# Optimization experiments

Measured on AMD Instinct MI355X. Metric: run time of the kernel, lower is better.

Reference implementation:

```python
import jax, jax.numpy as jnp
import numpy as np

NH = 8
DIM = 512
NP = 1024
MNP = 4096
BS = 4
TOPK = 32


def setup_inputs() -> dict:
    key = jax.random.key(0)
    ks = jax.random.split(key, 10)
    q = jax.random.normal(ks[0], (NP, BS, DIM), dtype=jnp.float32)
    k = jax.random.normal(ks[1], (MNP, BS, DIM), dtype=jnp.float32)
    v = jax.random.normal(ks[2], (MNP, BS, DIM), dtype=jnp.float32)
    rns_indices = jax.random.randint(ks[3], (BS, NP, TOPK), 0, MNP)
    s = 0.02
    W1 = jax.random.normal(ks[4], (DIM, DIM), dtype=jnp.float32) * s
    b1 = jnp.zeros((DIM,), dtype=jnp.float32)
    W2 = jax.random.normal(ks[5], (DIM, DIM), dtype=jnp.float32) * s
    b2 = jnp.zeros((DIM,), dtype=jnp.float32)
    W3 = jax.random.normal(ks[6], (DIM, DIM), dtype=jnp.float32) * s
    b3 = jnp.zeros((DIM,), dtype=jnp.float32)
    return {"q": q, "k": k, "v": v, "rns_indices": rns_indices,
            "W1": W1, "b1": b1, "W2": W2, "b2": b2, "W3": W3, "b3": b3}


def reference(q, k, v, rns_indices, W1, b1, W2, b2, W3, b3):
    np_, bs, dim = q.shape
    mnp = k.shape[0]
    nh = NH
    dh = dim // nh
    # seq-first -> batch-first, linear projections (torch Linear: x @ W.T + b)
    qh = (jnp.einsum('nbd,ed->bne', q, W1) + b1).reshape(bs, np_, nh, dh)
    kh = (jnp.einsum('mbd,ed->bme', k, W2) + b2).reshape(bs, mnp, nh, dh)
    vh = (jnp.einsum('mbd,ed->bme', v, W3) + b3).reshape(bs, mnp, nh, dh)
    # dense scores: [bs, nh, np, mnp]
    w = jnp.einsum('bnhd,bmhd->bhnm', qh, kh) / jnp.sqrt(jnp.asarray(dh, w_dtype := qh.dtype))
    # scatter-built neighbor mask: [bs, np, mnp] (shared across heads)
    b_idx = jnp.arange(bs)[:, None, None]
    n_idx = jnp.arange(np_)[None, :, None]
    mask = jnp.zeros((bs, np_, mnp), dtype=w.dtype).at[b_idx, n_idx, rns_indices].set(1.0)
    mask = mask[:, None, :, :]  # broadcast over heads
    w = w * mask + (-1e9) * (1.0 - mask)
    w = jax.nn.softmax(w, axis=3)
    out = jnp.einsum('bhnm,bmhd->nbhd', w, vh).reshape(np_, bs, dim)
    return out
```

## Files before the change

kernel.cpp:

```cpp
#include <hip/hip_runtime.h>
#include <hip/hip_bf16.h>
#include <stdint.h>

#define NH   8
#define DIM  512
#define NP   1024
#define MNP  4096
#define BS   4
#define TOPK 32
#define DH   64

typedef __attribute__((ext_vector_type(8))) short bf16x8;
typedef __attribute__((ext_vector_type(4))) float f32x4;

__device__ __forceinline__ unsigned short f2bf(float f) {
    union { float f; unsigned u; } x; x.f = f;
    unsigned r = x.u + 0x7FFFu + ((x.u >> 16) & 1u);
    return (unsigned short)(r >> 16);
}
__device__ __forceinline__ float bf2f(unsigned short h) {
    union { unsigned u; float f; } x; x.u = ((unsigned)h) << 16;
    return x.f;
}

__global__ void cvt_f32_bf16(const float* __restrict__ src,
                             unsigned short* __restrict__ dst, int n) {
    int i = (blockIdx.x * blockDim.x + threadIdx.x) * 4;
    if (i + 3 < n) {
        float4 v = *(const float4*)(src + i);
        ushort4 o;
        o.x = f2bf(v.x); o.y = f2bf(v.y); o.z = f2bf(v.z); o.w = f2bf(v.w);
        *(ushort4*)(dst + i) = o;
    } else {
        for (int j = i; j < n; j++) dst[j] = f2bf(src[j]);
    }
}

#define BM 128
#define BN 128
#define BK 64
#define LDT 72

__global__ __launch_bounds__(256, 2)
void proj_gemm(const float* __restrict__ A, const unsigned short* __restrict__ W,
               const float* __restrict__ bias, unsigned short* __restrict__ C) {
    __shared__ unsigned short As[BM * LDT];
    __shared__ unsigned short Bs[BN * LDT];

    const int tid  = threadIdx.x;
    const int bm   = blockIdx.y * BM;
    const int bn   = blockIdx.x * BN;
    const int wave = tid >> 6;
    const int lane = tid & 63;
    const int wm   = (wave & 1) * 64;
    const int wn   = (wave >> 1) * 64;
    const int l16  = lane & 15;
    const int quad = lane >> 4;

    f32x4 acc[4][4] = {};

    const int a_c4 = (tid & 15) * 4;
    const int a_r0 = tid >> 4;
    const int b_c8 = (tid & 7) * 8;
    const int b_r0 = tid >> 3;

    for (int k0 = 0; k0 < 512; k0 += BK) {
        __syncthreads();
#pragma unroll
        for (int rr = 0; rr < 8; rr++) {
            int row = a_r0 + rr * 16;
            float4 v = *(const float4*)(A + (size_t)(bm + row) * 512 + k0 + a_c4);
            ushort4 o;
            o.x = f2bf(v.x); o.y = f2bf(v.y); o.z = f2bf(v.z); o.w = f2bf(v.w);
            *(ushort4*)(&As[row * LDT + a_c4]) = o;
        }
#pragma unroll
        for (int rr = 0; rr < 4; rr++) {
            int row = b_r0 + rr * 32;
            uint4 p = *(const uint4*)(W + (size_t)(bn + row) * 512 + k0 + b_c8);
            *(uint4*)(&Bs[row * LDT + b_c8]) = p;
        }
        __syncthreads();
#pragma unroll
        for (int kk = 0; kk < BK; kk += 32) {
            bf16x8 af[4], bfr[4];
#pragma unroll
            for (int i = 0; i < 4; i++) {
                af[i]  = *(const bf16x8*)(&As[(wm + i * 16 + l16) * LDT + kk + quad * 8]);
                bfr[i] = *(const bf16x8*)(&Bs[(wn + i * 16 + l16) * LDT + kk + quad * 8]);
            }
#pragma unroll
            for (int i = 0; i < 4; i++)
#pragma unroll
                for (int j = 0; j < 4; j++)
                    acc[i][j] = __builtin_amdgcn_mfma_f32_16x16x32_bf16(
                        af[i], bfr[j], acc[i][j], 0, 0, 0);
        }
    }
#pragma unroll
    for (int i = 0; i < 4; i++) {
        int row = bm + wm + i * 16 + quad * 4;
#pragma unroll
        for (int j = 0; j < 4; j++) {
            int col = bn + wn + j * 16 + l16;
            float bv = bias[col];
#pragma unroll
            for (int r = 0; r < 4; r++)
                C[(size_t)(row + r) * 512 + col] = f2bf(acc[i][j][r] + bv);
        }
    }
}

__global__ __launch_bounds__(256)
void attn_kernel(const unsigned short* __restrict__ Qh,
                 const unsigned short* __restrict__ Kh,
                 const unsigned short* __restrict__ Vh,
                 const int* __restrict__ rns,
                 float* __restrict__ out) {
    __shared__ float sq[NH * 72];
    __shared__ int   sidx[TOPK];
    __shared__ int   srow[TOPK];
    __shared__ float sval[TOPK];
    __shared__ float ss[TOPK][NH];
    __shared__ float sw[TOPK][NH];

    const int bid = blockIdx.x;
    const int n = bid >> 2;
    const int b = bid & 3;
    const int tid = threadIdx.x;

    if (tid < TOPK) {
        int mi = rns[((b * NP + n) * TOPK) + tid];
        sidx[tid] = mi;
        srow[tid] = (mi * BS + b) * DIM;
    }
    {
        const unsigned short* qrow = Qh + (size_t)(n * BS + b) * DIM;
        unsigned int u = *(const unsigned int*)(qrow + tid * 2);
        int e0 = tid * 2;
        sq[(e0 >> 6) * 72 + (e0 & 63)]     = bf2f((unsigned short)(u & 0xffff));
        sq[(e0 >> 6) * 72 + ((e0 + 1) & 63)] = bf2f((unsigned short)(u >> 16));
    }
    __syncthreads();
    if (tid < TOPK) {
        float v = 1.0f;
        int me = sidx[tid];
        for (int j = 0; j < tid; j++)
            if (sidx[j] == me) v = 0.0f;
        sval[tid] = v;
    }
    __syncthreads();
    {
        const int i = tid >> 3;
        const int h = tid & 7;
        const unsigned short* krow = Kh + srow[i] + h * DH;
        const float* qh = sq + h * 72;
        float acc = 0.f;
#pragma unroll
        for (int d = 0; d < DH; d += 8) {
            uint4 kv = *(const uint4*)(krow + d);
            acc += qh[d + 0] * bf2f((unsigned short)(kv.x & 0xffff))
                 + qh[d + 1] * bf2f((unsigned short)(kv.x >> 16))
                 + qh[d + 2] * bf2f((unsigned short)(kv.y & 0xffff))
                 + qh[d + 3] * bf2f((unsigned short)(kv.y >> 16))
                 + qh[d + 4] * bf2f((unsigned short)(kv.z & 0xffff))
                 + qh[d + 5] * bf2f((unsigned short)(kv.z >> 16))
                 + qh[d + 6] * bf2f((unsigned short)(kv.w & 0xffff))
                 + qh[d + 7] * bf2f((unsigned short)(kv.w >> 16));
        }
        ss[i][h] = (sval[i] > 0.f) ? acc * 0.125f : -1e30f;
    }
    __syncthreads();
    if (tid < NH) {
        const int h = tid;
        float m = -1e30f;
        for (int i = 0; i < TOPK; i++) m = fmaxf(m, ss[i][h]);
        float s = 0.f;
        for (int i = 0; i < TOPK; i++) {
            float e = __expf(ss[i][h] - m);
            sw[i][h] = e; s += e;
        }
        float inv = 1.0f / s;
        for (int i = 0; i < TOPK; i++) sw[i][h] *= inv;
    }
    __syncthreads();
    {
        const int e0 = tid * 2;
        const int h = e0 >> 6;
        float a0 = 0.f, a1 = 0.f;
#pragma unroll 8
        for (int i = 0; i < TOPK; i++) {
            float w = sw[i][h];
            unsigned int vv = *(const unsigned int*)(Vh + srow[i] + e0);
            a0 += w * bf2f((unsigned short)(vv & 0xffff));
            a1 += w * bf2f((unsigned short)(vv >> 16));
        }
        float2* o = (float2*)(out + (size_t)(n * BS + b) * DIM + e0);
        *o = make_float2(a0, a1);
    }
}

extern "C" void kernel_launch(void* const* d_in, const int* in_sizes, int n_in,
                              void* d_out, int out_size, void* d_ws, size_t ws_size,
                              hipStream_t stream) {
    const float* q  = (const float*)d_in[0];
    const float* k  = (const float*)d_in[1];
    const float* v  = (const float*)d_in[2];
    const int* rns  = (const int*)d_in[3];
    const float* W1 = (const float*)d_in[4];
    const float* b1 = (const float*)d_in[5];
    const float* W2 = (const float*)d_in[6];
    const float* b2 = (const float*)d_in[7];
    const float* W3 = (const float*)d_in[8];
    const float* b3 = (const float*)d_in[9];
    float* out = (float*)d_out;

    unsigned short* ws  = (unsigned short*)d_ws;
    unsigned short* Wb1 = ws;
    unsigned short* Wb2 = Wb1 + 262144;
    unsigned short* Wb3 = Wb2 + 262144;
    unsigned short* Qh  = Wb3 + 262144;
    unsigned short* Kh  = Qh  + 2097152;
    unsigned short* Vh  = Kh  + 8388608;

    cvt_f32_bf16<<<256, 256, 0, stream>>>(W1, Wb1, 262144);
    cvt_f32_bf16<<<256, 256, 0, stream>>>(W2, Wb2, 262144);
    cvt_f32_bf16<<<256, 256, 0, stream>>>(W3, Wb3, 262144);

    dim3 blk(256);
    proj_gemm<<<dim3(4, 32),  blk, 0, stream>>>(q, Wb1, b1, Qh);
    proj_gemm<<<dim3(4, 128), blk, 0, stream>>>(k, Wb2, b2, Kh);
    proj_gemm<<<dim3(4, 128), blk, 0, stream>>>(v, Wb3, b3, Vh);

    attn_kernel<<<NP * BS, 256, 0, stream>>>(Qh, Kh, Vh, rns, out);
}
```

Before: 204.3 us.

## Pre-convert activations to bf16, batch projections, async LDS loads, shuffle softmax

Measured after the change: 198.7 us. 1.03x faster.

```diff
diff --git a/kernel.cpp b/kernel.cpp
--- a/kernel.cpp
+++ b/kernel.cpp
@@ -1,5 +1,4 @@
 #include <hip/hip_runtime.h>
-#include <hip/hip_bf16.h>
 #include <stdint.h>
 
 #define NH   8
@@ -10,46 +9,64 @@
 #define TOPK 32
 #define DH   64
 
+typedef unsigned short u16;
 typedef __attribute__((ext_vector_type(8))) short bf16x8;
 typedef __attribute__((ext_vector_type(4))) float f32x4;
 
-__device__ __forceinline__ unsigned short f2bf(float f) {
+__device__ __forceinline__ u16 f2bf(float f) {
     union { float f; unsigned u; } x; x.f = f;
     unsigned r = x.u + 0x7FFFu + ((x.u >> 16) & 1u);
-    return (unsigned short)(r >> 16);
-}
-__device__ __forceinline__ float bf2f(unsigned short h) {
+    return (u16)(r >> 16);
+}
+__device__ __forceinline__ float bf2f(u16 h) {
     union { unsigned u; float f; } x; x.u = ((unsigned)h) << 16;
     return x.f;
 }
 
-__global__ void cvt_f32_bf16(const float* __restrict__ src,
-                             unsigned short* __restrict__ dst, int n) {
-    int i = (blockIdx.x * blockDim.x + threadIdx.x) * 4;
-    if (i + 3 < n) {
-        float4 v = *(const float4*)(src + i);
-        ushort4 o;
-        o.x = f2bf(v.x); o.y = f2bf(v.y); o.z = f2bf(v.z); o.w = f2bf(v.w);
-        *(ushort4*)(dst + i) = o;
+__device__ __forceinline__ void async16(const void* g, void* l) {
+    __builtin_amdgcn_global_load_lds(
+        (const __attribute__((address_space(1))) unsigned int*)g,
+        (__attribute__((address_space(3))) unsigned int*)l, 16, 0, 0);
+}
+
+__global__ void cvt_all(const float* __restrict__ W1, const float* __restrict__ W2,
+                        const float* __restrict__ W3, const float* __restrict__ q,
+                        const float* __restrict__ k,  const float* __restrict__ v,
+                        u16* __restrict__ wall, u16* __restrict__ act) {
+    size_t i = ((size_t)blockIdx.x * 256 + threadIdx.x) * 4;
+    const float* s; u16* d;
+    if (i < 786432) {
+        d = wall + i;
+        s = (i < 262144) ? W1 + i : (i < 524288) ? W2 + (i - 262144) : W3 + (i - 524288);
     } else {
-        for (int j = i; j < n; j++) dst[j] = f2bf(src[j]);
-    }
-}
-
-#define BM 128
-#define BN 128
-#define BK 64
-#define LDT 72
+        size_t j = i - 786432;
+        d = act + j;
+        s = (j < 2097152) ? q + j : (j < 10485760) ? k + (j - 2097152) : v + (j - 10485760);
+    }
+    float4 val = *(const float4*)s;
+    ushort4 o;
+    o.x = f2bf(val.x); o.y = f2bf(val.y); o.z = f2bf(val.z); o.w = f2bf(val.w);
+    *(ushort4*)d = o;
+}
 
 __global__ __launch_bounds__(256, 2)
-void proj_gemm(const float* __restrict__ A, const unsigned short* __restrict__ W,
-               const float* __restrict__ bias, unsigned short* __restrict__ C) {
-    __shared__ unsigned short As[BM * LDT];
-    __shared__ unsigned short Bs[BN * LDT];
+void proj_gemm(const u16* __restrict__ act, const u16* __restrict__ wall,
+               const float* __restrict__ b1, const float* __restrict__ b2,
+               const float* __restrict__ b3, u16* __restrict__ outall) {
+    __shared__ u16 As[128 * 64];
+    __shared__ u16 Bs[128 * 64];
+
+    const int z = blockIdx.z;
+    if (z == 0 && blockIdx.y >= 32) return;
+    const size_t aoff = (z == 0) ? 0u : (z == 1) ? 2097152u : 10485760u;
+    const u16* A = act + aoff;
+    const u16* W = wall + (size_t)z * 262144;
+    const float* bias = (z == 0) ? b1 : (z == 1) ? b2 : b3;
+    u16* C = outall + aoff;
 
     const int tid  = threadIdx.x;
-    const int bm   = blockIdx.y * BM;
-    const int bn   = blockIdx.x * BN;
+    const int bm   = blockIdx.y * 128;
+    const int bn   = blockIdx.x * 128;
     const int wave = tid >> 6;
     const int lane = tid & 63;
     const int wm   = (wave & 1) * 64;
@@ -57,37 +74,29 @@
     const int l16  = lane & 15;
     const int quad = lane >> 4;
 
+    const int srow = lane >> 3;
+    const int scol = (lane & 7) * 8;
+
     f32x4 acc[4][4] = {};
 
-    const int a_c4 = (tid & 15) * 4;
-    const int a_r0 = tid >> 4;
-    const int b_c8 = (tid & 7) * 8;
-    const int b_r0 = tid >> 3;
-
-    for (int k0 = 0; k0 < 512; k0 += BK) {
+    for (int k0 = 0; k0 < 512; k0 += 64) {
         __syncthreads();
 #pragma unroll
-        for (int rr = 0; rr < 8; rr++) {
-            int row = a_r0 + rr * 16;
-            float4 v = *(const float4*)(A + (size_t)(bm + row) * 512 + k0 + a_c4);
-            ushort4 o;
-            o.x = f2bf(v.x); o.y = f2bf(v.y); o.z = f2bf(v.z); o.w = f2bf(v.w);
-            *(ushort4*)(&As[row * LDT + a_c4]) = o;
-        }
-#pragma unroll
-        for (int rr = 0; rr < 4; rr++) {
-            int row = b_r0 + rr * 32;
-            uint4 p = *(const uint4*)(W + (size_t)(bn + row) * 512 + k0 + b_c8);
-            *(uint4*)(&Bs[row * LDT + b_c8]) = p;
+        for (int r = 0; r < 4; r++) {
+            int row = wave * 32 + r * 8;
+            async16(A + (size_t)(bm + row + srow) * 512 + k0 + scol,
+                    &As[row * 64 + lane * 8]);
+            async16(W + (size_t)(bn + row + srow) * 512 + k0 + scol,
+                    &Bs[row * 64 + lane * 8]);
         }
         __syncthreads();
 #pragma unroll
-        for (int kk = 0; kk < BK; kk += 32) {
+        for (int kk = 0; kk < 64; kk += 32) {
             bf16x8 af[4], bfr[4];
 #pragma unroll
             for (int i = 0; i < 4; i++) {
-                af[i]  = *(const bf16x8*)(&As[(wm + i * 16 + l16) * LDT + kk + quad * 8]);
-                bfr[i] = *(const bf16x8*)(&Bs[(wn + i * 16 + l16) * LDT + kk + quad * 8]);
+                af[i]  = *(const bf16x8*)(&As[(wm + i * 16 + l16) * 64 + kk + quad * 8]);
+                bfr[i] = *(const bf16x8*)(&Bs[(wn + i * 16 + l16) * 64 + kk + quad * 8]);
             }
 #pragma unroll
             for (int i = 0; i < 4; i++)
@@ -112,22 +121,21 @@
 }
 
 __global__ __launch_bounds__(256)
-void attn_kernel(const unsigned short* __restrict__ Qh,
-                 const unsigned short* __restrict__ Kh,
-                 const unsigned short* __restrict__ Vh,
-                 const int* __restrict__ rns,
+void attn_kernel(const u16* __restrict__ Qh, const u16* __restrict__ Kh,
+                 const u16* __restrict__ Vh, const int* __restrict__ rns,
                  float* __restrict__ out) {
     __shared__ float sq[NH * 72];
     __shared__ int   sidx[TOPK];
     __shared__ int   srow[TOPK];
     __shared__ float sval[TOPK];
-    __shared__ float ss[TOPK][NH];
-    __shared__ float sw[TOPK][NH];
+    __shared__ float ss[TOPK][9];
+    __shared__ float sw[TOPK][9];
 
     const int bid = blockIdx.x;
     const int n = bid >> 2;
     const int b = bid & 3;
     const int tid = threadIdx.x;
+    const int lane = tid & 63;
 
     if (tid < TOPK) {
         int mi = rns[((b * NP + n) * TOPK) + tid];
@@ -135,11 +143,11 @@
         srow[tid] = (mi * BS + b) * DIM;
     }
     {
-        const unsigned short* qrow = Qh + (size_t)(n * BS + b) * DIM;
+        const u16* qrow = Qh + (size_t)(n * BS + b) * DIM;
         unsigned int u = *(const unsigned int*)(qrow + tid * 2);
         int e0 = tid * 2;
-        sq[(e0 >> 6) * 72 + (e0 & 63)]     = bf2f((unsigned short)(u & 0xffff));
-        sq[(e0 >> 6) * 72 + ((e0 + 1) & 63)] = bf2f((unsigned short)(u >> 16));
+        sq[(e0 >> 6) * 72 + (e0 & 63)]       = bf2f((u16)(u & 0xffff));
+        sq[(e0 >> 6) * 72 + ((e0 + 1) & 63)] = bf2f((u16)(u >> 16));
     }
     __syncthreads();
     if (tid < TOPK) {
@@ -153,50 +161,64 @@
     {
         const int i = tid >> 3;
         const int h = tid & 7;
-        const unsigned short* krow = Kh + srow[i] + h * DH;
+        const u16* krow = Kh + srow[i] + h * DH;
         const float* qh = sq + h * 72;
         float acc = 0.f;
 #pragma unroll
         for (int d = 0; d < DH; d += 8) {
             uint4 kv = *(const uint4*)(krow + d);
-            acc += qh[d + 0] * bf2f((unsigned short)(kv.x & 0xffff))
-                 + qh[d + 1] * bf2f((unsigned short)(kv.x >> 16))
-                 + qh[d + 2] * bf2f((unsigned short)(kv.y & 0xffff))
-                 + qh[d + 3] * bf2f((unsigned short)(kv.y >> 16))
-                 + qh[d + 4] * bf2f((unsigned short)(kv.z & 0xffff))
-                 + qh[d + 5] * bf2f((unsigned short)(kv.z >> 16))
-                 + qh[d + 6] * bf2f((unsigned short)(kv.w & 0xffff))
-                 + qh[d + 7] * bf2f((unsigned short)(kv.w >> 16));
+            float4 qa = *(const float4*)(qh + d);
+            float4 qb = *(const float4*)(qh + d + 4);
+            acc += qa.x * bf2f((u16)(kv.x & 0xffff)) + qa.y * bf2f((u16)(kv.x >> 16))
+                 + qa.z * bf2f((u16)(kv.y & 0xffff)) + qa.w * bf2f((u16)(kv.y >> 16))
+                 + qb.x * bf2f((u16)(kv.z & 0xffff)) + qb.y * bf2f((u16)(kv.z >> 16))
+                 + qb.z * bf2f((u16)(kv.w & 0xffff)) + qb.w * bf2f((u16)(kv.w >> 16));
         }
         ss[i][h] = (sval[i] > 0.f) ? acc * 0.125f : -1e30f;
     }
     __syncthreads();
-    if (tid < NH) {
-        const int h = tid;
-        float m = -1e30f;
-        for (int i = 0; i < TOPK; i++) m = fmaxf(m, ss[i][h]);
-        float s = 0.f;
-        for (int i = 0; i < TOPK; i++) {
-            float e = __expf(ss[i][h] - m);
-            sw[i][h] = e; s += e;
-        }
-        float inv = 1.0f / s;
-        for (int i = 0; i < TOPK; i++) sw[i][h] *= inv;
-    }
-    __syncthreads();
-    {
-        const int e0 = tid * 2;
-        const int h = e0 >> 6;
-        float a0 = 0.f, a1 = 0.f;
-#pragma unroll 8
-        for (int i = 0; i < TOPK; i++) {
+    {
+        const int h = tid >> 5;
+        const int i = tid & 31;
+        float val = ss[i][h];
+        float m = val;
+#pragma unroll
+        for (int msk = 1; msk < 32; msk <<= 1) m = fmaxf(m, __shfl_xor(m, msk, 64));
+        float e = __expf(val - m);
+        float s = e;
+#pragma unroll
+        for (int msk = 1; msk < 32; msk <<= 1) s += __shfl_xor(s, msk, 64);
+        sw[i][h] = e / s;
+    }
+    __syncthreads();
+    {
+        const int wv   = tid >> 6;
+        const int part = lane & 3;
+        const int e8   = (wv * 16 + (lane >> 2)) * 8;
+        const int h    = e8 >> 6;
+        float a[8] = {0, 0, 0, 0, 0, 0, 0, 0};
+#pragma unroll
+        for (int j = 0; j < 8; j++) {
+            int i = part * 8 + j;
             float w = sw[i][h];
-            unsigned int vv = *(const unsigned int*)(Vh + srow[i] + e0);
-            a0 += w * bf2f((unsigned short)(vv & 0xffff));
-            a1 += w * bf2f((unsigned short)(vv >> 16));
-        }
-        float2* o = (float2*)(out + (size_t)(n * BS + b) * DIM + e0);
-        *o = make_float2(a0, a1);
+            uint4 vv = *(const uint4*)(Vh + srow[i] + e8);
+            a[0] += w * bf2f((u16)(vv.x & 0xffff)); a[1] += w * bf2f((u16)(vv.x >> 16));
+            a[2] += w * bf2f((u16)(vv.y & 0xffff)); a[3] += w * bf2f((u16)(vv.y >> 16));
+            a[4] += w * bf2f((u16)(vv.z & 0xffff)); a[5] += w * bf2f((u16)(vv.z >> 16));
+            a[6] += w * bf2f((u16)(vv.w & 0xffff)); a[7] += w * bf2f((u16)(vv.w >> 16));
+        }
+#pragma unroll
+        for (int j = 0; j < 8; j++) {
+            a[j] += __shfl_xor(a[j], 1, 64);
+            a[j] += __shfl_xor(a[j], 2, 64);
+        }
+        if (part == 0) {
+            float* op = out + (size_t)(n * BS + b) * DIM + e8;
+            float4 o0 = {a[0], a[1], a[2], a[3]};
+            float4 o1 = {a[4], a[5], a[6], a[7]};
+            *(float4*)op = o0;
+            *((float4*)op + 1) = o1;
+        }
     }
 }
 
@@ -215,22 +237,15 @@
     const float* b3 = (const float*)d_in[9];
     float* out = (float*)d_out;
 
-    unsigned short* ws  = (unsigned short*)d_ws;
-    unsigned short* Wb1 = ws;
-    unsigned short* Wb2 = Wb1 + 262144;
-    unsigned short* Wb3 = Wb2 + 262144;
-    unsigned short* Qh  = Wb3 + 262144;
-    unsigned short* Kh  = Qh  + 2097152;
-    unsigned short* Vh  = Kh  + 8388608;
-
-    cvt_f32_bf16<<<256, 256, 0, stream>>>(W1, Wb1, 262144);
-    cvt_f32_bf16<<<256, 256, 0, stream>>>(W2, Wb2, 262144);
-    cvt_f32_bf16<<<256, 256, 0, stream>>>(W3, Wb3, 262144);
-
-    dim3 blk(256);
-    proj_gemm<<<dim3(4, 32),  blk, 0, stream>>>(q, Wb1, b1, Qh);
-    proj_gemm<<<dim3(4, 128), blk, 0, stream>>>(k, Wb2, b2, Kh);
-    proj_gemm<<<dim3(4, 128), blk, 0, stream>>>(v, Wb3, b3, Vh);
-
+    u16* ws   = (u16*)d_ws;
+    u16* wall = ws;
+    u16* act  = wall + 786432;
+    u16* proj = act + 18874368;
+    u16* Qh = proj;
+    u16* Kh = proj + 2097152;
+    u16* Vh = proj + 10485760;
+
+    cvt_all<<<19200, 256, 0, stream>>>(W1, W2, W3, q, k, v, wall, act);
+    proj_gemm<<<dim3(4, 128, 3), 256, 0, stream>>>(act, wall, b1, b2, b3, proj);
     attn_kernel<<<NP * BS, 256, 0, stream>>>(Qh, Kh, Vh, rns, out);
 }
```
